# Kernel optimization log

Measured on AMD Instinct MI355X. Metric: run time of the kernel, lower is better.

Reference implementation:

```python
import jax, jax.numpy as jnp
import numpy as np

# Canonical DAG: L topological levels of N nodes each; every node in level l>0
# has K predecessors in level l-1, each edge carrying a scalar weight.
# Input nodes (level 0) take x columns directly (no activation), matching the
# torch module. Output = activations of the (sorted) last-level nodes.

B, N, K, L = 1024, 5000, 16, 10  # batch, nodes/level, fan-in, levels
NEG_SLOPE = 0.1                  # LeakyReLU(0.1) as in the module


def setup_inputs() -> dict:
    key = jax.random.key(0)
    k_x, k_s, k_w, k_b = jax.random.split(key, 4)
    x = jax.random.normal(k_x, (B, N), dtype=jnp.float32)
    # predecessor indices into the previous level, per level 1..L-1
    src_idx = jax.random.randint(k_s, (L - 1, N, K), 0, N)
    # scalar edge weights and node biases ~ N(0, 0.1), as in __init__
    weights = jax.random.normal(k_w, (L - 1, N, K), dtype=jnp.float32) * 0.1
    biases = jax.random.normal(k_b, (L - 1, N), dtype=jnp.float32) * 0.1
    return {"x": x, "src_idx": src_idx, "weights": weights, "biases": biases}


def reference(x, src_idx, weights, biases):
    b, n = x.shape
    k = src_idx.shape[-1]

    def level(act, params):
        s, w, bias = params  # s,w: [N,K], bias: [N]
        # gather predecessor activations: [B, N, K]
        gathered = jnp.take(act, s.reshape(-1), axis=1).reshape(b, n, k)
        # weighted sum over predecessors + bias, then LeakyReLU(0.1)
        pre = jnp.einsum('bnk,nk->bn', gathered, w) + bias
        return jax.nn.leaky_relu(pre, NEG_SLOPE), None

    out, _ = jax.lax.scan(level, x, (src_idx, weights, biases))
    return out  # [B, N] activations of output nodes (sorted order)
```

## Files before the change

### kernel.cpp

```cpp
#include <hip/hip_runtime.h>


#define TB 1024
#define TN 5000
#define TK 16
#define TLV 9
#define CPG 4
#define NG  (TB / CPG)
#define LT  1024
#define PEL (TN * TK)

#define SLOTP 5056
#define PSTRIDE (SLOTP * 8)
#define WOFF_IT 8192

typedef unsigned int u32;
typedef unsigned short u16;
typedef _Float16 h2 __attribute__((ext_vector_type(2)));

__device__ __forceinline__ h2 u2h(u32 v) { return __builtin_bit_cast(h2, v); }
__device__ __forceinline__ u32 h2u(h2 h) { return __builtin_bit_cast(u32, h); }
__device__ __forceinline__ u32 packf(float a, float b) {
    h2 h; h.x = (_Float16)a; h.y = (_Float16)b;
    return h2u(h);
}

__global__ __launch_bounds__(256) void k_pack(
    const int* __restrict__ idx, const float* __restrict__ w,
    const float* __restrict__ biases,
    u32* __restrict__ pe, u32* __restrict__ b2)
{
    const int j = blockIdx.x * 256 + threadIdx.x;
    if (j < TLV * TN * TK) {
        const int l = j / (TN * TK);
        const u32 s = (u32)idx[j];
        h2 hw; hw.x = (_Float16)w[j]; hw.y = (_Float16)0.0f;
        pe[j] = ((u32)(l & 1) * (u32)SLOTP + s) | (h2u(hw) << 16);
    }
    if (j < TLV * TN) {
        const float b = biases[j];
        b2[j] = packf(b, b);
    }
}


#define PREF(S, LL, IT) do {                                                  \
    const size_t _n = (size_t)(LL) * TN + (size_t)(t + (IT) * LT);            \
    const uint4* _p = reinterpret_cast<const uint4*>(pe + _n * TK);           \
    S##a = _p[0]; S##b = _p[1]; S##c = _p[2]; S##d = _p[3];                   \
    S##i = b2[_n];                                                            \
} while (0)

#define EDGE(EV) do {                                                         \
    const u32 _e   = (EV);                                                    \
    const u32 _off = (_e & 0xffffu) << 3;              \
    const uint2 _av = *reinterpret_cast<const uint2*>(lds + _off);            \
    asm("v_pk_fma_f16 %0, %1, %2, %0 op_sel:[1,0,0] op_sel_hi:[1,1,1]"        \
        : "+v"(a01) : "v"(_e), "v"(_av.x));                                   \
    asm("v_pk_fma_f16 %0, %1, %2, %0 op_sel:[1,0,0] op_sel_hi:[1,1,1]"        \
        : "+v"(a23) : "v"(_e), "v"(_av.y));                                   \
} while (0)

#define COMP(S, WBASE, IT) do {                                               \
    u32 a01 = S##i, a23 = S##i;                      \
    EDGE(S##a.x); EDGE(S##a.y); EDGE(S##a.z); EDGE(S##a.w);                   \
    EDGE(S##b.x); EDGE(S##b.y); EDGE(S##b.z); EDGE(S##b.w);                   \
    EDGE(S##c.x); EDGE(S##c.y); EDGE(S##c.z); EDGE(S##c.w);                   \
    EDGE(S##d.x); EDGE(S##d.y); EDGE(S##d.z); EDGE(S##d.w);                   \
    h2 A = u2h(a01), Bv = u2h(a23);                                           \
    h2 tenth; tenth.x = (_Float16)0.1f; tenth.y = (_Float16)0.1f;             \
    A  = __builtin_elementwise_max(A,  A  * tenth);                           \
    Bv = __builtin_elementwise_max(Bv, Bv * tenth);                           \
    uint2 _r; _r.x = h2u(A); _r.y = h2u(Bv);                                  \
    *reinterpret_cast<uint2*>(lds + (WBASE) + (IT) * WOFF_IT) = _r;           \
} while (0)

#define LVL(LL, S0, S1, WBASE, LAST) do {                                     \
    PREF(S1, (LL), 1); COMP(S0, WBASE, 0);                                    \
    PREF(S0, (LL), 2); COMP(S1, WBASE, 1);                                    \
    PREF(S1, (LL), 3); COMP(S0, WBASE, 2);                                    \
    if (t4) PREF(S0, (LL), 4);                                                \
    COMP(S1, WBASE, 3);                                                       \
    if (!(LAST)) PREF(S1, (LL) + 1, 0);                                       \
    if (t4) COMP(S0, WBASE, 4);                                               \
    __syncthreads();                                                          \
} while (0)

__global__ __launch_bounds__(LT) void k_fused(
    const float* __restrict__ x,
    float* __restrict__ out,
    const u32* __restrict__ pe,
    const u32* __restrict__ b2)
{
    __shared__ char lds[2 * PSTRIDE];
    const int g = blockIdx.x;
    const int t = threadIdx.x;
    const bool t4 = t < (TN - 4 * LT);
    const u32 woO = (u32)t * 8u;
    const u32 woE = (u32)(SLOTP + t) * 8u;

    uint4 Pa, Pb, Pc, Pd; u32 Pi;
    uint4 Qa, Qb, Qc, Qd; u32 Qi;

    PREF(P, 0, 0);

    {
        const float* xp0 = x + (size_t)(g * CPG + 0) * TN;
        const float* xp1 = x + (size_t)(g * CPG + 1) * TN;
        const float* xp2 = x + (size_t)(g * CPG + 2) * TN;
        const float* xp3 = x + (size_t)(g * CPG + 3) * TN;
        #pragma unroll
        for (int it = 0; it < 4; ++it) {
            const int n = t + it * LT;
            uint2 v;
            v.x = packf(xp0[n], xp1[n]);
            v.y = packf(xp2[n], xp3[n]);
            *reinterpret_cast<uint2*>(lds + woO + it * WOFF_IT) = v;
        }
        if (t4) {
            const int n = t + 4 * LT;
            uint2 v;
            v.x = packf(xp0[n], xp1[n]);
            v.y = packf(xp2[n], xp3[n]);
            *reinterpret_cast<uint2*>(lds + woO + 4 * WOFF_IT) = v;
        }
    }
    __syncthreads();

    #pragma unroll 1
    for (int lp = 0; lp < 4; ++lp) {
        LVL(2 * lp,     P, Q, woE, false);
        LVL(2 * lp + 1, Q, P, woO, false);
    }
    LVL(8, P, Q, woE, true);

    {
        float* op0 = out + (size_t)(g * CPG + 0) * TN;
        float* op1 = out + (size_t)(g * CPG + 1) * TN;
        float* op2 = out + (size_t)(g * CPG + 2) * TN;
        float* op3 = out + (size_t)(g * CPG + 3) * TN;
        #pragma unroll
        for (int it = 0; it < 4; ++it) {
            const int n = t + it * LT;
            const uint2 v = *reinterpret_cast<const uint2*>(lds + woE + it * WOFF_IT);
            h2 h;
            h = u2h(v.x); op0[n] = (float)h.x; op1[n] = (float)h.y;
            h = u2h(v.y); op2[n] = (float)h.x; op3[n] = (float)h.y;
        }
        if (t4) {
            const int n = t + 4 * LT;
            const uint2 v = *reinterpret_cast<const uint2*>(lds + woE + 4 * WOFF_IT);
            h2 h;
            h = u2h(v.x); op0[n] = (float)h.x; op1[n] = (float)h.y;
            h = u2h(v.y); op2[n] = (float)h.x; op3[n] = (float)h.y;
        }
    }
}

extern "C" void kernel_launch(void* const* d_in, const int* in_sizes, int n_in,
                              void* d_out, int out_size, void* d_ws, size_t ws_size,
                              hipStream_t stream)
{
    const float* x       = (const float*)d_in[0];
    const int*   src_idx = (const int*)  d_in[1];
    const float* weights = (const float*)d_in[2];
    const float* biases  = (const float*)d_in[3];
    float* out = (float*)d_out;

    u32* pe = (u32*)d_ws;
    u32* b2 = pe + (size_t)TLV * TN * TK;

    {
        const int ne = TLV * TN * TK;
        hipLaunchKernelGGL(k_pack, dim3((ne + 255) / 256), dim3(256), 0, stream,
                           src_idx, weights, biases, pe, b2);
    }
    hipLaunchKernelGGL(k_fused, dim3(NG), dim3(LT), 0, stream,
                       x, out, pe, b2);
}
```

Baseline: 135.0 us.

## Process two nodes per thread with interleaved gathers, drop software prefetch

Each level now has every thread handle two nodes at once, interleaving their LDS gathers and packed FMAs to raise instruction-level parallelism. This replaces the explicit register double-buffered prefetch of edge records across levels. The packed edge offset is premultiplied by 8, and the slot selection moves to a per-level read base, so the kernel no longer shifts or adds a per-level slot offset for each edge. All levels are fully unrolled. Dropping the cross-level prefetch can expose global load latency at each level start, and two nodes in flight per thread raises register pressure at 1024 threads per block.

```diff
diff --git a/kernel.cpp b/kernel.cpp
--- a/kernel.cpp
+++ b/kernel.cpp
@@ -10,9 +10,7 @@
 #define LT  1024
 #define PEL (TN * TK)
 
-#define SLOTP 5056
-#define PSTRIDE (SLOTP * 8)
-#define WOFF_IT 8192
+#define PSTRIDE 40448
 
 typedef unsigned int u32;
 typedef unsigned short u16;
@@ -32,10 +30,9 @@
 {
     const int j = blockIdx.x * 256 + threadIdx.x;
     if (j < TLV * TN * TK) {
-        const int l = j / (TN * TK);
         const u32 s = (u32)idx[j];
         h2 hw; hw.x = (_Float16)w[j]; hw.y = (_Float16)0.0f;
-        pe[j] = ((u32)(l & 1) * (u32)SLOTP + s) | (h2u(hw) << 16);
+        pe[j] = (s * 8u) | (h2u(hw) << 16);
     }
     if (j < TLV * TN) {
         const float b = biases[j];
@@ -44,45 +41,79 @@
 }
 
 
-#define PREF(S, LL, IT) do {                                                  \
-    const size_t _n = (size_t)(LL) * TN + (size_t)(t + (IT) * LT);            \
-    const uint4* _p = reinterpret_cast<const uint4*>(pe + _n * TK);           \
-    S##a = _p[0]; S##b = _p[1]; S##c = _p[2]; S##d = _p[3];                   \
-    S##i = b2[_n];                                                            \
-} while (0)
-
-#define EDGE(EV) do {                                                         \
-    const u32 _e   = (EV);                                                    \
-    const u32 _off = (_e & 0xffffu) << 3;              \
-    const uint2 _av = *reinterpret_cast<const uint2*>(lds + _off);            \
-    asm("v_pk_fma_f16 %0, %1, %2, %0 op_sel:[1,0,0] op_sel_hi:[1,1,1]"        \
-        : "+v"(a01) : "v"(_e), "v"(_av.x));                                   \
-    asm("v_pk_fma_f16 %0, %1, %2, %0 op_sel:[1,0,0] op_sel_hi:[1,1,1]"        \
-        : "+v"(a23) : "v"(_e), "v"(_av.y));                                   \
-} while (0)
-
-#define COMP(S, WBASE, IT) do {                                               \
-    u32 a01 = S##i, a23 = S##i;                      \
-    EDGE(S##a.x); EDGE(S##a.y); EDGE(S##a.z); EDGE(S##a.w);                   \
-    EDGE(S##b.x); EDGE(S##b.y); EDGE(S##b.z); EDGE(S##b.w);                   \
-    EDGE(S##c.x); EDGE(S##c.y); EDGE(S##c.z); EDGE(S##c.w);                   \
-    EDGE(S##d.x); EDGE(S##d.y); EDGE(S##d.z); EDGE(S##d.w);                   \
-    h2 A = u2h(a01), Bv = u2h(a23);                                           \
-    h2 tenth; tenth.x = (_Float16)0.1f; tenth.y = (_Float16)0.1f;             \
-    A  = __builtin_elementwise_max(A,  A  * tenth);                           \
-    Bv = __builtin_elementwise_max(Bv, Bv * tenth);                           \
-    uint2 _r; _r.x = h2u(A); _r.y = h2u(Bv);                                  \
-    *reinterpret_cast<uint2*>(lds + (WBASE) + (IT) * WOFF_IT) = _r;           \
-} while (0)
-
-#define LVL(LL, S0, S1, WBASE, LAST) do {                                     \
-    PREF(S1, (LL), 1); COMP(S0, WBASE, 0);                                    \
-    PREF(S0, (LL), 2); COMP(S1, WBASE, 1);                                    \
-    PREF(S1, (LL), 3); COMP(S0, WBASE, 2);                                    \
-    if (t4) PREF(S0, (LL), 4);                                                \
-    COMP(S1, WBASE, 3);                                                       \
-    if (!(LAST)) PREF(S1, (LL) + 1, 0);                                       \
-    if (t4) COMP(S0, WBASE, 4);                                               \
+#define EDGE2(E0, E1, RP) do {                                                \
+    const u32 _o0 = (E0) & 0xffffu;                      \
+    const u32 _o1 = (E1) & 0xffffu;                                           \
+    const uint2 _a = *reinterpret_cast<const uint2*>(lds + (RP) + _o0);       \
+    const uint2 _b = *reinterpret_cast<const uint2*>(lds + (RP) + _o1);       \
+    asm("v_pk_fma_f16 %0, %1, %2, %0 op_sel:[1,0,0] op_sel_hi:[1,1,1]"        \
+        : "+v"(x01) : "v"(E0), "v"(_a.x));                                    \
+    asm("v_pk_fma_f16 %0, %1, %2, %0 op_sel:[1,0,0] op_sel_hi:[1,1,1]"        \
+        : "+v"(x23) : "v"(E0), "v"(_a.y));                                    \
+    asm("v_pk_fma_f16 %0, %1, %2, %0 op_sel:[1,0,0] op_sel_hi:[1,1,1]"        \
+        : "+v"(y01) : "v"(E1), "v"(_b.x));                                    \
+    asm("v_pk_fma_f16 %0, %1, %2, %0 op_sel:[1,0,0] op_sel_hi:[1,1,1]"        \
+        : "+v"(y23) : "v"(E1), "v"(_b.y));                                    \
+} while (0)
+
+#define LRELU(acc) do {                                                       \
+    h2 _v = u2h(acc);                                                         \
+    h2 _t; _t.x = (_Float16)0.1f; _t.y = (_Float16)0.1f;                      \
+    _v = __builtin_elementwise_max(_v, _v * _t);                              \
+    acc = h2u(_v);                                                            \
+} while (0)
+
+#define PAIR(RP, WP, IT) do {                                                 \
+    const size_t _n0 = (size_t)(t + (IT) * LT);                               \
+    const uint4* _p0 = reinterpret_cast<const uint4*>(ep_l + _n0 * TK);       \
+    const uint4* _p1 = reinterpret_cast<const uint4*>(ep_l + (_n0 + LT) * TK);\
+    const uint4 A0 = _p0[0], A1 = _p0[1], A2 = _p0[2], A3 = _p0[3];           \
+    const uint4 B0 = _p1[0], B1 = _p1[1], B2 = _p1[2], B3 = _p1[3];           \
+    u32 x01 = b_l[_n0];      u32 x23 = x01;                                   \
+    u32 y01 = b_l[_n0 + LT]; u32 y23 = y01;                                   \
+    EDGE2(A0.x, B0.x, RP); EDGE2(A0.y, B0.y, RP);                             \
+    EDGE2(A0.z, B0.z, RP); EDGE2(A0.w, B0.w, RP);                             \
+    EDGE2(A1.x, B1.x, RP); EDGE2(A1.y, B1.y, RP);                             \
+    EDGE2(A1.z, B1.z, RP); EDGE2(A1.w, B1.w, RP);                             \
+    EDGE2(A2.x, B2.x, RP); EDGE2(A2.y, B2.y, RP);                             \
+    EDGE2(A2.z, B2.z, RP); EDGE2(A2.w, B2.w, RP);                             \
+    EDGE2(A3.x, B3.x, RP); EDGE2(A3.y, B3.y, RP);                             \
+    EDGE2(A3.z, B3.z, RP); EDGE2(A3.w, B3.w, RP);                             \
+    LRELU(x01); LRELU(x23); LRELU(y01); LRELU(y23);                           \
+    uint2 _rx; _rx.x = x01; _rx.y = x23;                                      \
+    uint2 _ry; _ry.x = y01; _ry.y = y23;                                      \
+    *reinterpret_cast<uint2*>(lds + (WP) + (IT) * 8192 + wv) = _rx;           \
+    *reinterpret_cast<uint2*>(lds + (WP) + ((IT) + 1) * 8192 + wv) = _ry;     \
+} while (0)
+
+#define SINGLE(RP, WP, IT) do {                                               \
+    const size_t _n0 = (size_t)(t + (IT) * LT);                               \
+    const uint4* _p0 = reinterpret_cast<const uint4*>(ep_l + _n0 * TK);       \
+    const uint4 A0 = _p0[0], A1 = _p0[1], A2 = _p0[2], A3 = _p0[3];           \
+    u32 x01 = b_l[_n0]; u32 x23 = x01;                                        \
+    const u32 es[TK] = {A0.x, A0.y, A0.z, A0.w, A1.x, A1.y, A1.z, A1.w,       \
+                        A2.x, A2.y, A2.z, A2.w, A3.x, A3.y, A3.z, A3.w};      \
+    _Pragma("unroll")                                                         \
+    for (int k = 0; k < TK; ++k) {                                            \
+        const u32 _e  = es[k];                                                \
+        const u32 _o  = _e & 0xffffu;                                         \
+        const uint2 _a = *reinterpret_cast<const uint2*>(lds + (RP) + _o);    \
+        asm("v_pk_fma_f16 %0, %1, %2, %0 op_sel:[1,0,0] op_sel_hi:[1,1,1]"    \
+            : "+v"(x01) : "v"(_e), "v"(_a.x));                                \
+        asm("v_pk_fma_f16 %0, %1, %2, %0 op_sel:[1,0,0] op_sel_hi:[1,1,1]"    \
+            : "+v"(x23) : "v"(_e), "v"(_a.y));                                \
+    }                                                                         \
+    LRELU(x01); LRELU(x23);                                                   \
+    uint2 _rx; _rx.x = x01; _rx.y = x23;                                      \
+    *reinterpret_cast<uint2*>(lds + (WP) + (IT) * 8192 + wv) = _rx;           \
+} while (0)
+
+#define LEVEL(LIDX, RP, WP) do {                                              \
+    const u32* ep_l = pe + (size_t)(LIDX) * PEL;                              \
+    const u32* b_l  = b2 + (size_t)(LIDX) * TN;                               \
+    PAIR(RP, WP, 0);                                                          \
+    PAIR(RP, WP, 2);                                                          \
+    if (t4) SINGLE(RP, WP, 4);                                                \
     __syncthreads();                                                          \
 } while (0)
 
@@ -92,17 +123,12 @@
     const u32* __restrict__ pe,
     const u32* __restrict__ b2)
 {
-    __shared__ char lds[2 * PSTRIDE];
+    __shared__ uint2 sbuf[2 * (PSTRIDE / 8)];
+    char* lds = reinterpret_cast<char*>(sbuf);
     const int g = blockIdx.x;
     const int t = threadIdx.x;
     const bool t4 = t < (TN - 4 * LT);
-    const u32 woO = (u32)t * 8u;
-    const u32 woE = (u32)(SLOTP + t) * 8u;
-
-    uint4 Pa, Pb, Pc, Pd; u32 Pi;
-    uint4 Qa, Qb, Qc, Qd; u32 Qi;
-
-    PREF(P, 0, 0);
+    const u32 wv = (u32)t * 8u;
 
     {
         const float* xp0 = x + (size_t)(g * CPG + 0) * TN;
@@ -115,24 +141,27 @@
             uint2 v;
             v.x = packf(xp0[n], xp1[n]);
             v.y = packf(xp2[n], xp3[n]);
-            *reinterpret_cast<uint2*>(lds + woO + it * WOFF_IT) = v;
+            *reinterpret_cast<uint2*>(lds + it * 8192 + wv) = v;
         }
         if (t4) {
             const int n = t + 4 * LT;
             uint2 v;
             v.x = packf(xp0[n], xp1[n]);
             v.y = packf(xp2[n], xp3[n]);
-            *reinterpret_cast<uint2*>(lds + woO + 4 * WOFF_IT) = v;
+            *reinterpret_cast<uint2*>(lds + 4 * 8192 + wv) = v;
         }
     }
     __syncthreads();
 
-    #pragma unroll 1
-    for (int lp = 0; lp < 4; ++lp) {
-        LVL(2 * lp,     P, Q, woE, false);
-        LVL(2 * lp + 1, Q, P, woO, false);
-    }
-    LVL(8, P, Q, woE, true);
+    LEVEL(0, 0,       PSTRIDE);
+    LEVEL(1, PSTRIDE, 0);
+    LEVEL(2, 0,       PSTRIDE);
+    LEVEL(3, PSTRIDE, 0);
+    LEVEL(4, 0,       PSTRIDE);
+    LEVEL(5, PSTRIDE, 0);
+    LEVEL(6, 0,       PSTRIDE);
+    LEVEL(7, PSTRIDE, 0);
+    LEVEL(8, 0,       PSTRIDE);
 
     {
         float* op0 = out + (size_t)(g * CPG + 0) * TN;
@@ -142,14 +171,16 @@
         #pragma unroll
         for (int it = 0; it < 4; ++it) {
             const int n = t + it * LT;
-            const uint2 v = *reinterpret_cast<const uint2*>(lds + woE + it * WOFF_IT);
+            const uint2 v =
+                *reinterpret_cast<const uint2*>(lds + PSTRIDE + it * 8192 + wv);
             h2 h;
             h = u2h(v.x); op0[n] = (float)h.x; op1[n] = (float)h.y;
             h = u2h(v.y); op2[n] = (float)h.x; op3[n] = (float)h.y;
         }
         if (t4) {
             const int n = t + 4 * LT;
-            const uint2 v = *reinterpret_cast<const uint2*>(lds + woE + 4 * WOFF_IT);
+            const uint2 v =
+                *reinterpret_cast<const uint2*>(lds + PSTRIDE + 4 * 8192 + wv);
             h2 h;
             h = u2h(v.x); op0[n] = (float)h.x; op1[n] = (float)h.y;
             h = u2h(v.y); op2[n] = (float)h.x; op3[n] = (float)h.y;
```

Measured after the change: 138.1 us. 1.02x slower.
